# Kernel optimization log

Measured on AMD Instinct MI355X. Metric: run time of the kernel, lower is better.

The kernel has to match this reference:

```python
import jax, jax.numpy as jnp
import numpy as np

# Model/config dims (Llama-3-8B style attention, GQA 32q/8kv)
B, S, HID = 4, 512, 4096
NH, NKV, D = 32, 8, 128
CAP = 2048          # KV cache capacity
MAXPOS = 2048       # max_position_embeddings
START = 1024        # kvcache_start_index (uniform across batch -> static masking)
EPS = 1e-6
QK_SCALE = 1.0 / float(D) ** 0.5
NEG = -1e9


def setup_inputs() -> dict:
    key = jax.random.key(0)
    ks = jax.random.split(key, 8)
    w = 0.02  # weight init scale
    return {
        'hidden_states': jax.random.normal(ks[0], (B, S, HID), jnp.float32),
        'k_cache': jax.random.normal(ks[1], (B, NKV, CAP, D), jnp.float32),
        'v_cache': jax.random.normal(ks[2], (B, NKV, CAP, D), jnp.float32),
        'rope_rotary_cos_sin': jax.random.uniform(ks[3], (B, MAXPOS, D), jnp.float32),
        'context_lengths': jnp.full((B,), S, jnp.int32),
        'kvcache_start_index': jnp.full((B,), START, jnp.int32),
        'Wq': jax.random.normal(ks[4], (HID, NH * D), jnp.float32) * w,
        'Wk': jax.random.normal(ks[5], (HID, NKV * D), jnp.float32) * w,
        'Wv': jax.random.normal(ks[6], (HID, NKV * D), jnp.float32) * w,
        'Wo': jax.random.normal(ks[7], (NH * D, HID), jnp.float32) * w,
        'q_norm_w': jnp.ones((D,), jnp.float32),
        'k_norm_w': jnp.ones((D,), jnp.float32),
    }


def _rmsnorm(x, w):
    # per-head RMSNorm over head_dim (Qwen3-style QK norm)
    return x * jax.lax.rsqrt(jnp.mean(x * x, axis=-1, keepdims=True) + EPS) * w


def _apply_rope(x, cos, sin, pos):
    # x: [B,H,S,D]; cos/sin: [MAXPOS, D/2]; pos: [B,S]
    c = cos[pos][:, None, :, :]  # [B,1,S,D/2]
    s = sin[pos][:, None, :, :]
    x1, x2 = jnp.split(x, 2, axis=-1)
    return jnp.concatenate([x1 * c - x2 * s, x2 * c + x1 * s], axis=-1)


def reference(hidden_states, k_cache, v_cache, rope_rotary_cos_sin,
              context_lengths, kvcache_start_index,
              Wq, Wk, Wv, Wo, q_norm_w, k_norm_w):
    b, s, _ = hidden_states.shape
    # fused QKV projection
    q = (hidden_states @ Wq).reshape(b, s, NH, D)
    k = (hidden_states @ Wk).reshape(b, s, NKV, D)
    v = (hidden_states @ Wv).reshape(b, s, NKV, D)
    # QK norm
    q = _rmsnorm(q, q_norm_w)
    k = _rmsnorm(k, k_norm_w)
    # [B,H,S,D]
    q = q.transpose(0, 2, 1, 3)
    k = k.transpose(0, 2, 1, 3)
    v = v.transpose(0, 2, 1, 3)
    # RoPE tables: first half cos, second half sin; batch dim 0 only
    half = D // 2
    cos = rope_rotary_cos_sin[0, :, :half]
    sin = rope_rotary_cos_sin[0, :, half:]
    pos = kvcache_start_index[:, None] + jnp.arange(s, dtype=kvcache_start_index.dtype)[None, :]
    q = _apply_rope(q, cos, sin, pos)
    k = _apply_rope(k, cos, sin, pos)
    # KV cache update: write new k/v at per-batch start index
    def upd(cache, new, st):  # cache [H,CAP,D], new [H,S,D]
        return jax.lax.dynamic_update_slice(cache, new, (0, st, 0))
    present_k = jax.vmap(upd)(k_cache, k, kvcache_start_index)
    present_v = jax.vmap(upd)(v_cache, v, kvcache_start_index)
    # GQA: expand kv heads to attention heads
    g = NH // NKV
    kf = jnp.repeat(present_k, g, axis=1)  # [B,NH,CAP,D]
    vf = jnp.repeat(present_v, g, axis=1)
    # scaled attention over cache; mask cols beyond absolute query position
    scores = jnp.einsum('bhsd,bhtd->bhst', q * QK_SCALE, kf)
    col = jnp.arange(CAP, dtype=pos.dtype)
    allowed = col[None, None, :] <= pos[:, :, None]        # [B,S,CAP]
    scores = jnp.where(allowed[:, None, :, :], scores, NEG)
    attn = jax.nn.softmax(scores, axis=-1)
    out = jnp.einsum('bhst,bhtd->bhsd', attn, vf)
    out = out.transpose(0, 2, 1, 3).reshape(b, s, NH * D)
    out = out @ Wo
    return out, present_k, present_v
```

## Files before the change

### kernel.cpp

```cpp
#include <hip/hip_runtime.h>
#include <hip/hip_bf16.h>
#include <cstdint>

#define Bsz   4
#define Ssz   512
#define HIDsz 4096
#define NHsz  32
#define NKVsz 8
#define Dsz   128
#define CAPsz 2048
#define EPSf  1e-6f
#define QK_SCALEf 0.08838834764831845f

typedef __attribute__((ext_vector_type(8))) short short8;
typedef __attribute__((ext_vector_type(4))) float f32x4;

__device__ __forceinline__ unsigned short f2bf(float x) {
    unsigned u = __float_as_uint(x);
    return (unsigned short)((u + 0x7fffu + ((u >> 16) & 1u)) >> 16);
}

__device__ __forceinline__ void gload16(const void* g, void* l) {
    __builtin_amdgcn_global_load_lds(
        (const __attribute__((address_space(1))) unsigned int*)g,
        (__attribute__((address_space(3))) unsigned int*)l, 16, 0, 0);
}

__global__ __launch_bounds__(256) void convert_bf16_kernel(
    const float* __restrict__ in, unsigned short* __restrict__ out, int n4)
{
    int i = blockIdx.x * blockDim.x + threadIdx.x;
    if (i < n4) {
        float4 v = ((const float4*)in)[i];
        ushort4 o;
        o.x = f2bf(v.x); o.y = f2bf(v.y); o.z = f2bf(v.z); o.w = f2bf(v.w);
        ((ushort4*)out)[i] = o;
    }
}

__global__ __launch_bounds__(256) void transpose_bf16_kernel(
    const float* __restrict__ W, unsigned short* __restrict__ Wt, int K, int N)
{
    __shared__ float tile[64][65];
    const int k0 = blockIdx.y * 64, n0 = blockIdx.x * 64;
    const int t = threadIdx.x;
    const int tr = t >> 4, tc4 = (t & 15) * 4;
#pragma unroll
    for (int i = 0; i < 4; i++) {
        int r = tr + i * 16;
        float4 v = *(const float4*)(W + (size_t)(k0 + r) * N + n0 + tc4);
        tile[r][tc4 + 0] = v.x; tile[r][tc4 + 1] = v.y;
        tile[r][tc4 + 2] = v.z; tile[r][tc4 + 3] = v.w;
    }
    __syncthreads();
#pragma unroll
    for (int i = 0; i < 4; i++) {
        int nr = tr + i * 16;
        ushort4 o;
        o.x = f2bf(tile[tc4 + 0][nr]);
        o.y = f2bf(tile[tc4 + 1][nr]);
        o.z = f2bf(tile[tc4 + 2][nr]);
        o.w = f2bf(tile[tc4 + 3][nr]);
        *(ushort4*)(Wt + (size_t)(n0 + nr) * K + k0 + tc4) = o;
    }
}

__global__ __launch_bounds__(256) void transpose_v_kernel(
    const float* __restrict__ V, unsigned short* __restrict__ Vt)
{
    __shared__ float tile[64][65];
    const int c0 = blockIdx.x * 64, d0 = blockIdx.y * 64, bk = blockIdx.z;
    const int t = threadIdx.x;
    const int tr = t >> 4, tc4 = (t & 15) * 4;
    const float* base = V + (size_t)bk * CAPsz * Dsz;
#pragma unroll
    for (int i = 0; i < 4; i++) {
        int r = tr + i * 16;
        float4 v = *(const float4*)(base + (size_t)(c0 + r) * Dsz + d0 + tc4);
        tile[r][tc4 + 0] = v.x; tile[r][tc4 + 1] = v.y;
        tile[r][tc4 + 2] = v.z; tile[r][tc4 + 3] = v.w;
    }
    __syncthreads();
    unsigned short* ob = Vt + (size_t)bk * Dsz * CAPsz;
#pragma unroll
    for (int i = 0; i < 4; i++) {
        int dr = tr + i * 16;
        ushort4 o;
        o.x = f2bf(tile[tc4 + 0][dr]);
        o.y = f2bf(tile[tc4 + 1][dr]);
        o.z = f2bf(tile[tc4 + 2][dr]);
        o.w = f2bf(tile[tc4 + 3][dr]);
        *(ushort4*)(ob + (size_t)(d0 + dr) * CAPsz + c0 + tc4) = o;
    }
}

__global__ __launch_bounds__(256, 2) void gemm_bf16_kernel(
    const unsigned short* __restrict__ A,
    const unsigned short* __restrict__ Bt,
    float* __restrict__ C, int M, int N, int K)
{
    __shared__ __align__(16) unsigned short As[128 * 64];
    __shared__ __align__(16) unsigned short Bs[128 * 64];
    const int t    = threadIdx.x;
    const int lane = t & 63, wv = t >> 6;
    const int m0 = blockIdx.y * 128, n0 = blockIdx.x * 128;
    const int rw = (wv & 1) * 64, cw = (wv >> 1) * 64;

    f32x4 acc[4][4];
#pragma unroll
    for (int r = 0; r < 4; r++)
#pragma unroll
        for (int c = 0; c < 4; c++) acc[r][c] = (f32x4){0.f, 0.f, 0.f, 0.f};

    const int arow = lane >> 3;
    const int acol = (lane & 7) * 8;
    const int fr = lane & 15, fq = (lane >> 4) * 8;

    for (int k0 = 0; k0 < K; k0 += 64) {
        __syncthreads();
#pragma unroll
        for (int i = 0; i < 4; i++) {
            int ro = (i * 4 + wv) * 8;
            gload16(A  + (size_t)(m0 + ro + arow) * K + k0 + acol, As + (size_t)ro * 64);
            gload16(Bt + (size_t)(n0 + ro + arow) * K + k0 + acol, Bs + (size_t)ro * 64);
        }
        __syncthreads();
#pragma unroll
        for (int kk = 0; kk < 2; kk++) {
            short8 af[4], bfr[4];
#pragma unroll
            for (int r = 0; r < 4; r++)
                af[r] = *(const short8*)&As[(rw + r * 16 + fr) * 64 + kk * 32 + fq];
#pragma unroll
            for (int c = 0; c < 4; c++)
                bfr[c] = *(const short8*)&Bs[(cw + c * 16 + fr) * 64 + kk * 32 + fq];
#pragma unroll
            for (int r = 0; r < 4; r++)
#pragma unroll
                for (int c = 0; c < 4; c++)
                    acc[r][c] = __builtin_amdgcn_mfma_f32_16x16x32_bf16(
                        af[r], bfr[c], acc[r][c], 0, 0, 0);
        }
    }

#pragma unroll
    for (int r = 0; r < 4; r++) {
#pragma unroll
        for (int c = 0; c < 4; c++) {
            int col = n0 + cw + c * 16 + (lane & 15);
#pragma unroll
            for (int reg = 0; reg < 4; reg++) {
                int row = m0 + rw + r * 16 + (lane >> 4) * 4 + reg;
                C[(size_t)row * N + col] = acc[r][c][reg];
            }
        }
    }
}

__global__ __launch_bounds__(256, 2) void gemm_qkv_kernel(
    const unsigned short* __restrict__ A,
    const unsigned short* __restrict__ Bt,
    float* __restrict__ Cq,
    float* __restrict__ Ck,
    float* __restrict__ Cv,
    const int* __restrict__ start_idx)
{
    __shared__ __align__(16) unsigned short As[128 * 64];
    __shared__ __align__(16) unsigned short Bs[128 * 64];
    const int t    = threadIdx.x;
    const int lane = t & 63, wv = t >> 6;
    const int m0 = blockIdx.y * 128, n0 = blockIdx.x * 128;
    const int rw = (wv & 1) * 64, cw = (wv >> 1) * 64;

    f32x4 acc[4][4];
#pragma unroll
    for (int r = 0; r < 4; r++)
#pragma unroll
        for (int c = 0; c < 4; c++) acc[r][c] = (f32x4){0.f, 0.f, 0.f, 0.f};

    const int arow = lane >> 3;
    const int acol = (lane & 7) * 8;
    const int fr = lane & 15, fq = (lane >> 4) * 8;

    for (int k0 = 0; k0 < HIDsz; k0 += 64) {
        __syncthreads();
#pragma unroll
        for (int i = 0; i < 4; i++) {
            int ro = (i * 4 + wv) * 8;
            gload16(A  + (size_t)(m0 + ro + arow) * HIDsz + k0 + acol, As + (size_t)ro * 64);
            gload16(Bt + (size_t)(n0 + ro + arow) * HIDsz + k0 + acol, Bs + (size_t)ro * 64);
        }
        __syncthreads();
#pragma unroll
        for (int kk = 0; kk < 2; kk++) {
            short8 af[4], bfr[4];
#pragma unroll
            for (int r = 0; r < 4; r++)
                af[r] = *(const short8*)&As[(rw + r * 16 + fr) * 64 + kk * 32 + fq];
#pragma unroll
            for (int c = 0; c < 4; c++)
                bfr[c] = *(const short8*)&Bs[(cw + c * 16 + fr) * 64 + kk * 32 + fq];
#pragma unroll
            for (int r = 0; r < 4; r++)
#pragma unroll
                for (int c = 0; c < 4; c++)
                    acc[r][c] = __builtin_amdgcn_mfma_f32_16x16x32_bf16(
                        af[r], bfr[c], acc[r][c], 0, 0, 0);
        }
    }

    const int pos0 = start_idx[m0 >> 9];
    const bool isQ = (n0 < 4096);
    const bool isK = (n0 >= 4096) && (n0 < 5120);
    float* dst = isK ? Ck : Cv;
    const int cbase = isK ? 4096 : 5120;
#pragma unroll
    for (int r = 0; r < 4; r++) {
#pragma unroll
        for (int c = 0; c < 4; c++) {
            int col = n0 + cw + c * 16 + (lane & 15);
#pragma unroll
            for (int reg = 0; reg < 4; reg++) {
                int row = m0 + rw + r * 16 + (lane >> 4) * 4 + reg;
                float val = acc[r][c][reg];
                if (isQ) {
                    Cq[(size_t)row * 4096 + col] = val;
                } else {
                    int cc = col - cbase;
                    int pos = pos0 + (row & (Ssz - 1));
                    int b = row >> 9;
                    dst[((size_t)(b * NKVsz + (cc >> 7)) * CAPsz + pos) * Dsz + (cc & 127)] = val;
                }
            }
        }
    }
}

__global__ __launch_bounds__(256) void rmsnorm_rope_kernel(
    float* __restrict__ X, unsigned short* __restrict__ Xbf,
    const float* __restrict__ w,
    const float* __restrict__ rope, const int* __restrict__ start_idx,
    int nheads, int mode)
{
    int gid   = blockIdx.x * blockDim.x + threadIdx.x;
    int wid   = gid >> 6;
    int lane  = threadIdx.x & 63;
    int token = wid / nheads;
    int h     = wid - token * nheads;
    int b = token >> 9, s = token & (Ssz - 1);
    int pos = start_idx[b] + s;
    float* row;
    if (mode == 0) row = X + (size_t)token * (nheads * Dsz) + h * Dsz;
    else           row = X + ((size_t)(b * nheads + h) * CAPsz + pos) * Dsz;

    float x1 = row[lane], x2 = row[lane + 64];
    float ss = x1 * x1 + x2 * x2;
#pragma unroll
    for (int off = 32; off > 0; off >>= 1) ss += __shfl_xor(ss, off);
    float rn  = rsqrtf(ss * (1.f / 128.f) + EPSf);
    float xn1 = x1 * rn * w[lane];
    float xn2 = x2 * rn * w[lane + 64];
    float c   = rope[(size_t)pos * Dsz + lane];
    float sn  = rope[(size_t)pos * Dsz + 64 + lane];
    float o1 = xn1 * c - xn2 * sn;
    float o2 = xn2 * c + xn1 * sn;
    if (mode == 0) {
        unsigned short* orow = Xbf + (size_t)token * (nheads * Dsz) + h * Dsz;
        orow[lane]      = f2bf(o1 * QK_SCALEf);
        orow[lane + 64] = f2bf(o2 * QK_SCALEf);
    } else {
        row[lane]      = o1;
        row[lane + 64] = o2;
    }
}

__global__ __launch_bounds__(256, 2) void attn_mfma_kernel(
    const unsigned short* __restrict__ Qbf,
    const unsigned short* __restrict__ Kbf,
    const unsigned short* __restrict__ Vtbf,
    unsigned short* __restrict__ O,
    const int* __restrict__ start_idx)
{
    __shared__ __align__(16) unsigned short Ks[64 * 128];
    __shared__ __align__(16) unsigned short Vs[128 * 64];
    __shared__ __align__(16) unsigned short Ps[4][32 * 72];

    const int t = threadIdx.x, lane = t & 63, wv = t >> 6;
    const int l15 = lane & 15, l4 = lane >> 4;
    const int qt = blockIdx.x, kv = blockIdx.y, b = blockIdx.z;
    const int h = kv * 4 + wv;
    const int s0 = qt * 32;
    const int start = start_idx[b];

    const int swz = (l15 & 7) << 3;

    short8 aq[2][4];
    const unsigned short* qb = Qbf + ((size_t)(b * Ssz + s0)) * HIDsz + h * Dsz;
#pragma unroll
    for (int m2 = 0; m2 < 2; m2++)
#pragma unroll
        for (int kq = 0; kq < 4; kq++)
            aq[m2][kq] = *(const short8*)(qb + (size_t)(m2 * 16 + l15) * HIDsz + kq * 32 + l4 * 8);

    f32x4 Oacc[2][8];
    float m_run[2][4], l_run[2][4];
#pragma unroll
    for (int m2 = 0; m2 < 2; m2++) {
#pragma unroll
        for (int nd = 0; nd < 8; nd++) Oacc[m2][nd] = (f32x4){0.f, 0.f, 0.f, 0.f};
#pragma unroll
        for (int r = 0; r < 4; r++) { m_run[m2][r] = -1e30f; l_run[m2][r] = 0.f; }
    }

    const unsigned short* kb = Kbf + (size_t)(b * NKVsz + kv) * CAPsz * Dsz;
    const unsigned short* vb = Vtbf + (size_t)(b * NKVsz + kv) * (size_t)Dsz * CAPsz;

    int t_hi = start + s0 + 31;
    if (t_hi > CAPsz - 1) t_hi = CAPsz - 1;

    int krow[4], vrow[4];
    unsigned short* kw[4];
    unsigned short* vw[4];
#pragma unroll
    for (int i = 0; i < 4; i++) {
        int kr = (i * 4 + wv) * 4 + l4;
        krow[i] = kr;
        kw[i] = &Ks[kr * 128 + ((l15 * 8) ^ ((kr & 7) << 3))];
        int vr = (i * 4 + wv) * 8 + (lane >> 3);
        vrow[i] = vr;
        vw[i] = &Vs[vr * 64 + (((lane & 7) * 8) ^ ((vr & 7) << 3))];
    }

    short8 kreg[4], vreg[4];
#pragma unroll
    for (int i = 0; i < 4; i++) {
        kreg[i] = *(const short8*)(kb + (size_t)krow[i] * Dsz + l15 * 8);
        vreg[i] = *(const short8*)(vb + (size_t)vrow[i] * CAPsz + (lane & 7) * 8);
    }

    for (int t0 = 0; t0 <= t_hi; t0 += 64) {
        asm volatile("s_waitcnt lgkmcnt(0)" ::: "memory");
        __builtin_amdgcn_s_barrier();
        __builtin_amdgcn_sched_barrier(0);

#pragma unroll
        for (int i = 0; i < 4; i++) *(short8*)kw[i] = kreg[i];
#pragma unroll
        for (int i = 0; i < 4; i++) *(short8*)vw[i] = vreg[i];

        if (t0 + 64 <= t_hi) {
            int tn = t0 + 64;
#pragma unroll
            for (int i = 0; i < 4; i++) {
                kreg[i] = *(const short8*)(kb + (size_t)(tn + krow[i]) * Dsz + l15 * 8);
                vreg[i] = *(const short8*)(vb + (size_t)vrow[i] * CAPsz + tn + (lane & 7) * 8);
            }
        }

        asm volatile("s_waitcnt lgkmcnt(0)" ::: "memory");
        __builtin_amdgcn_s_barrier();
        __builtin_amdgcn_sched_barrier(0);

        f32x4 Sacc[2][4];
#pragma unroll
        for (int m2 = 0; m2 < 2; m2++)
#pragma unroll
            for (int n = 0; n < 4; n++) Sacc[m2][n] = (f32x4){0.f, 0.f, 0.f, 0.f};
        __builtin_amdgcn_s_setprio(1);
#pragma unroll
        for (int kq = 0; kq < 4; kq++) {
            short8 bk[4];
#pragma unroll
            for (int n = 0; n < 4; n++)
                bk[n] = *(const short8*)&Ks[(n * 16 + l15) * 128 + ((kq * 32 + l4 * 8) ^ swz)];
#pragma unroll
            for (int m2 = 0; m2 < 2; m2++)
#pragma unroll
                for (int n = 0; n < 4; n++)
                    Sacc[m2][n] = __builtin_amdgcn_mfma_f32_16x16x32_bf16(
                        aq[m2][kq], bk[n], Sacc[m2][n], 0, 0, 0);
        }
        __builtin_amdgcn_s_setprio(0);

        bool need_mask = (t0 + 63) > (start + s0);
#pragma unroll
        for (int m2 = 0; m2 < 2; m2++) {
#pragma unroll
            for (int reg = 0; reg < 4; reg++) {
                int rloc = m2 * 16 + l4 * 4 + reg;
                int row_pos = start + s0 + rloc;
                float sv[4];
#pragma unroll
                for (int n = 0; n < 4; n++) {
                    sv[n] = Sacc[m2][n][reg];
                    if (need_mask && (t0 + n * 16 + l15 > row_pos)) sv[n] = -1e30f;
                }
                float mrow = fmaxf(fmaxf(sv[0], sv[1]), fmaxf(sv[2], sv[3]));
#pragma unroll
                for (int off = 1; off < 16; off <<= 1)
                    mrow = fmaxf(mrow, __shfl_xor(mrow, off));
                float m_new = fmaxf(m_run[m2][reg], mrow);
                float alpha = __expf(m_run[m2][reg] - m_new);
                float ps = 0.f;
#pragma unroll
                for (int n = 0; n < 4; n++) {
                    sv[n] = __expf(sv[n] - m_new);
                    ps += sv[n];
                }
#pragma unroll
                for (int off = 1; off < 16; off <<= 1)
                    ps += __shfl_xor(ps, off);
                l_run[m2][reg] = l_run[m2][reg] * alpha + ps;
                m_run[m2][reg] = m_new;
#pragma unroll
                for (int nd = 0; nd < 8; nd++) Oacc[m2][nd][reg] *= alpha;
#pragma unroll
                for (int n = 0; n < 4; n++)
                    Ps[wv][rloc * 72 + n * 16 + l15] = f2bf(sv[n]);
            }
        }

        __builtin_amdgcn_s_setprio(1);
#pragma unroll
        for (int kp = 0; kp < 2; kp++) {
            short8 ap[2];
#pragma unroll
            for (int m2 = 0; m2 < 2; m2++)
                ap[m2] = *(const short8*)&Ps[wv][(m2 * 16 + l15) * 72 + kp * 32 + l4 * 8];
#pragma unroll
            for (int nd = 0; nd < 8; nd++) {
                short8 bv = *(const short8*)&Vs[(nd * 16 + l15) * 64 + ((kp * 32 + l4 * 8) ^ swz)];
#pragma unroll
                for (int m2 = 0; m2 < 2; m2++)
                    Oacc[m2][nd] = __builtin_amdgcn_mfma_f32_16x16x32_bf16(
                        ap[m2], bv, Oacc[m2][nd], 0, 0, 0);
            }
        }
        __builtin_amdgcn_s_setprio(0);
    }

    unsigned short* ob = O + ((size_t)(b * Ssz + s0)) * HIDsz + h * Dsz;
#pragma unroll
    for (int m2 = 0; m2 < 2; m2++)
#pragma unroll
        for (int reg = 0; reg < 4; reg++) {
            int rloc = m2 * 16 + l4 * 4 + reg;
            float inv = 1.f / l_run[m2][reg];
#pragma unroll
            for (int nd = 0; nd < 8; nd++)
                ob[(size_t)rloc * HIDsz + nd * 16 + l15] = f2bf(Oacc[m2][nd][reg] * inv);
        }
}

extern "C" void kernel_launch(void* const* d_in, const int* in_sizes, int n_in,
                              void* d_out, int out_size, void* d_ws, size_t ws_size,
                              hipStream_t stream) {
    (void)in_sizes; (void)n_in; (void)out_size; (void)ws_size;
    const float* hidden    = (const float*)d_in[0];
    const float* k_cache   = (const float*)d_in[1];
    const float* v_cache   = (const float*)d_in[2];
    const float* rope      = (const float*)d_in[3];
    const int*   start_idx = (const int*)d_in[5];
    const float* Wq        = (const float*)d_in[6];
    const float* Wk        = (const float*)d_in[7];
    const float* Wv        = (const float*)d_in[8];
    const float* Wo        = (const float*)d_in[9];
    const float* q_norm_w  = (const float*)d_in[10];
    const float* k_norm_w  = (const float*)d_in[11];

    float* out   = (float*)d_out;
    float* out_k = out + (size_t)Bsz * Ssz * HIDsz;
    float* out_v = out_k + (size_t)Bsz * NKVsz * CAPsz * Dsz;

    char* ws = (char*)d_ws;
    float*          q_ws      = (float*)ws;
    unsigned short* Kbf       = (unsigned short*)ws;
    unsigned short* Vtbf      = (unsigned short*)(ws + (((size_t) 16) << 20));
    unsigned short* hidden_bf = (unsigned short*)(ws + (((size_t) 32) << 20));
    unsigned short* attn_bf   = (unsigned short*)(ws + (((size_t) 48) << 20));
    unsigned short* qbf       = (unsigned short*)(ws + (((size_t) 64) << 20));
    unsigned short* Wqkv_t    = (unsigned short*)(ws + (((size_t) 80) << 20));
    unsigned short* Wk_t      = Wqkv_t + (size_t)4096 * 4096;
    unsigned short* Wv_t      = Wqkv_t + (size_t)5120 * 4096;
    unsigned short* Wo_t      = Wqkv_t;

    const size_t cache_bytes = (size_t)Bsz * NKVsz * CAPsz * Dsz * sizeof(float);
    (void)hipMemcpyAsync(out_k, k_cache, cache_bytes, hipMemcpyDeviceToDevice, stream);
    (void)hipMemcpyAsync(out_v, v_cache, cache_bytes, hipMemcpyDeviceToDevice, stream);

    convert_bf16_kernel<<<8192, 256, 0, stream>>>(hidden, hidden_bf, 2048 * 4096 / 4);
    transpose_bf16_kernel<<<dim3(64, 64), 256, 0, stream>>>(Wq, Wqkv_t, HIDsz, NHsz * Dsz);
    transpose_bf16_kernel<<<dim3(16, 64), 256, 0, stream>>>(Wk, Wk_t, HIDsz, NKVsz * Dsz);
    transpose_bf16_kernel<<<dim3(16, 64), 256, 0, stream>>>(Wv, Wv_t, HIDsz, NKVsz * Dsz);

    gemm_qkv_kernel<<<dim3(48, 16), 256, 0, stream>>>(
        hidden_bf, Wqkv_t, q_ws, out_k, out_v, start_idx);

    rmsnorm_rope_kernel<<<16384, 256, 0, stream>>>(q_ws, qbf, q_norm_w, rope, start_idx, NHsz, 0);
    rmsnorm_rope_kernel<<<4096, 256, 0, stream>>>(out_k, nullptr, k_norm_w, rope, start_idx, NKVsz, 1);

    convert_bf16_kernel<<<8192, 256, 0, stream>>>(out_k, Kbf, Bsz * NKVsz * CAPsz * Dsz / 4);
    transpose_v_kernel<<<dim3(32, 2, 32), 256, 0, stream>>>(out_v, Vtbf);

    attn_mfma_kernel<<<dim3(16, NKVsz, Bsz), 256, 0, stream>>>(qbf, Kbf, Vtbf, attn_bf, start_idx);

    transpose_bf16_kernel<<<dim3(64, 64), 256, 0, stream>>>(Wo, Wo_t, NHsz * Dsz, HIDsz);
    gemm_bf16_kernel<<<dim3(32, 16), 256, 0, stream>>>(attn_bf, Wo_t, out, 2048, 4096, 4096);
}
```

Before: 673.3 us.

## Fuse QK RMSNorm and RoPE into QKV GEMM epilogue, skip unused cache regions

Moves the per-head RMSNorm and RoPE for Q and K into the QKV GEMM epilogue. A shared-memory reduction produces the row norms, and RoPE partners are swapped between waves through shared memory. Q is written directly as bf16 and K as both fp32 and bf16, which removes the fp32 Q round trip and the separate norm/rope kernels. The K bf16 conversion and the V transpose now skip cache positions the attention does not read, and the three weight transposes are merged into one launch. Occupancy hints are raised to 3 blocks. The epilogue now uses more shared memory and extra syncs, which may limit the higher occupancy target.

```diff
diff --git a/kernel.cpp b/kernel.cpp
--- a/kernel.cpp
+++ b/kernel.cpp
@@ -38,6 +38,20 @@
     }
 }
 
+__global__ __launch_bounds__(256) void convert_k_prefix_kernel(
+    const float* __restrict__ in, unsigned short* __restrict__ out,
+    const int* __restrict__ start_idx)
+{
+    int i = blockIdx.x * blockDim.x + threadIdx.x;
+    int pos = (i >> 5) & (CAPsz - 1);
+    int b   = i >> 19;
+    if (pos >= start_idx[b]) return;
+    float4 v = ((const float4*)in)[i];
+    ushort4 o;
+    o.x = f2bf(v.x); o.y = f2bf(v.y); o.z = f2bf(v.z); o.w = f2bf(v.w);
+    ((ushort4*)out)[i] = o;
+}
+
 __global__ __launch_bounds__(256) void transpose_bf16_kernel(
     const float* __restrict__ W, unsigned short* __restrict__ Wt, int K, int N)
 {
@@ -65,11 +79,47 @@
     }
 }
 
+__global__ __launch_bounds__(256) void transpose_wqkv_kernel(
+    const float* __restrict__ Wq, const float* __restrict__ Wk,
+    const float* __restrict__ Wv, unsigned short* __restrict__ Wt)
+{
+    __shared__ float tile[64][65];
+    const int nt = blockIdx.x;
+    const int k0 = blockIdx.y * 64;
+    const float* W; int srcN, c0;
+    if (nt < 64)      { W = Wq; srcN = 4096; c0 = nt * 64; }
+    else if (nt < 80) { W = Wk; srcN = 1024; c0 = (nt - 64) * 64; }
+    else              { W = Wv; srcN = 1024; c0 = (nt - 80) * 64; }
+    const int t = threadIdx.x;
+    const int tr = t >> 4, tc4 = (t & 15) * 4;
+#pragma unroll
+    for (int i = 0; i < 4; i++) {
+        int r = tr + i * 16;
+        float4 v = *(const float4*)(W + (size_t)(k0 + r) * srcN + c0 + tc4);
+        tile[r][tc4 + 0] = v.x; tile[r][tc4 + 1] = v.y;
+        tile[r][tc4 + 2] = v.z; tile[r][tc4 + 3] = v.w;
+    }
+    __syncthreads();
+    const int n0 = nt * 64;
+#pragma unroll
+    for (int i = 0; i < 4; i++) {
+        int nr = tr + i * 16;
+        ushort4 o;
+        o.x = f2bf(tile[tc4 + 0][nr]);
+        o.y = f2bf(tile[tc4 + 1][nr]);
+        o.z = f2bf(tile[tc4 + 2][nr]);
+        o.w = f2bf(tile[tc4 + 3][nr]);
+        *(ushort4*)(Wt + (size_t)(n0 + nr) * HIDsz + k0 + tc4) = o;
+    }
+}
+
 __global__ __launch_bounds__(256) void transpose_v_kernel(
-    const float* __restrict__ V, unsigned short* __restrict__ Vt)
+    const float* __restrict__ V, unsigned short* __restrict__ Vt,
+    const int* __restrict__ start_idx)
 {
     __shared__ float tile[64][65];
     const int c0 = blockIdx.x * 64, d0 = blockIdx.y * 64, bk = blockIdx.z;
+    if (c0 >= start_idx[bk >> 3] + Ssz) return;
     const int t = threadIdx.x;
     const int tr = t >> 4, tc4 = (t & 15) * 4;
     const float* base = V + (size_t)bk * CAPsz * Dsz;
@@ -94,7 +144,7 @@
     }
 }
 
-__global__ __launch_bounds__(256, 2) void gemm_bf16_kernel(
+__global__ __launch_bounds__(256, 3) void gemm_bf16_kernel(
     const unsigned short* __restrict__ A,
     const unsigned short* __restrict__ Bt,
     float* __restrict__ C, int M, int N, int K)
@@ -157,20 +207,27 @@
     }
 }
 
-__global__ __launch_bounds__(256, 2) void gemm_qkv_kernel(
+__global__ __launch_bounds__(256, 3) void gemm_qkv_kernel(
     const unsigned short* __restrict__ A,
     const unsigned short* __restrict__ Bt,
-    float* __restrict__ Cq,
+    unsigned short* __restrict__ Qout,
     float* __restrict__ Ck,
     float* __restrict__ Cv,
+    unsigned short* __restrict__ Kbf,
+    const float* __restrict__ rope,
+    const float* __restrict__ qw,
+    const float* __restrict__ knw,
     const int* __restrict__ start_idx)
 {
     __shared__ __align__(16) unsigned short As[128 * 64];
     __shared__ __align__(16) unsigned short Bs[128 * 64];
+    __shared__ float ssbuf[256];
+    __shared__ float xbuf[256 * 17];
     const int t    = threadIdx.x;
     const int lane = t & 63, wv = t >> 6;
     const int m0 = blockIdx.y * 128, n0 = blockIdx.x * 128;
     const int rw = (wv & 1) * 64, cw = (wv >> 1) * 64;
+    const int l15 = lane & 15, l4 = lane >> 4;
 
     f32x4 acc[4][4];
 #pragma unroll
@@ -180,7 +237,7 @@
 
     const int arow = lane >> 3;
     const int acol = (lane & 7) * 8;
-    const int fr = lane & 15, fq = (lane >> 4) * 8;
+    const int fr = l15, fq = l4 * 8;
 
     for (int k0 = 0; k0 < HIDsz; k0 += 64) {
         __syncthreads();
@@ -209,68 +266,101 @@
         }
     }
 
-    const int pos0 = start_idx[m0 >> 9];
+    const int m0b  = m0 & (Ssz - 1);
+    const int bat  = m0 >> 9;
+    const int pos0 = start_idx[bat];
+
+    if (n0 >= 5120) {
+#pragma unroll
+        for (int r = 0; r < 4; r++) {
+#pragma unroll
+            for (int c = 0; c < 4; c++) {
+                int cc = (n0 - 5120) + cw + c * 16 + l15;
+                int kvh = cc >> 7, d = cc & 127;
+#pragma unroll
+                for (int reg = 0; reg < 4; reg++) {
+                    int srow = rw + r * 16 + l4 * 4 + reg;
+                    int pos = pos0 + m0b + srow;
+                    Cv[((size_t)(bat * NKVsz + kvh) * CAPsz + pos) * Dsz + d] = acc[r][c][reg];
+                }
+            }
+        }
+        return;
+    }
+
     const bool isQ = (n0 < 4096);
-    const bool isK = (n0 >= 4096) && (n0 < 5120);
-    float* dst = isK ? Ck : Cv;
-    const int cbase = isK ? 4096 : 5120;
+    const float* w = isQ ? qw : knw;
+
+#pragma unroll
+    for (int r = 0; r < 4; r++)
+#pragma unroll
+        for (int reg = 0; reg < 4; reg++) {
+            float p = acc[r][0][reg] * acc[r][0][reg]
+                    + acc[r][1][reg] * acc[r][1][reg]
+                    + acc[r][2][reg] * acc[r][2][reg]
+                    + acc[r][3][reg] * acc[r][3][reg];
+#pragma unroll
+            for (int off = 1; off < 16; off <<= 1) p += __shfl_xor(p, off);
+            if (l15 == 0)
+                ssbuf[(rw + r * 16 + l4 * 4 + reg) * 2 + (cw >> 6)] = p;
+        }
+    __syncthreads();
+
+    float wv4[4];
+#pragma unroll
+    for (int c = 0; c < 4; c++) wv4[c] = w[cw + c * 16 + l15];
+
+    float rn[4][4];
+#pragma unroll
+    for (int r = 0; r < 4; r++)
+#pragma unroll
+        for (int reg = 0; reg < 4; reg++) {
+            int srow = rw + r * 16 + l4 * 4 + reg;
+            rn[r][reg] = rsqrtf((ssbuf[srow * 2] + ssbuf[srow * 2 + 1]) * (1.f / 128.f) + EPSf);
+        }
+
+    const int kvh = isQ ? 0 : ((n0 - 4096) >> 7);
+
 #pragma unroll
     for (int r = 0; r < 4; r++) {
-#pragma unroll
-        for (int c = 0; c < 4; c++) {
-            int col = n0 + cw + c * 16 + (lane & 15);
+        float xn[4][4];
+#pragma unroll
+        for (int c = 0; c < 4; c++)
 #pragma unroll
             for (int reg = 0; reg < 4; reg++) {
-                int row = m0 + rw + r * 16 + (lane >> 4) * 4 + reg;
-                float val = acc[r][c][reg];
+                xn[c][reg] = acc[r][c][reg] * rn[r][reg] * wv4[c];
+                xbuf[t * 17 + c * 4 + reg] = xn[c][reg];
+            }
+        __syncthreads();
+        float xp[4][4];
+#pragma unroll
+        for (int c = 0; c < 4; c++)
+#pragma unroll
+            for (int reg = 0; reg < 4; reg++)
+                xp[c][reg] = xbuf[(t ^ 128) * 17 + c * 4 + reg];
+
+#pragma unroll
+        for (int reg = 0; reg < 4; reg++) {
+            int srow = rw + r * 16 + l4 * 4 + reg;
+            int pos = pos0 + m0b + srow;
+            const float* rb = rope + (size_t)pos * Dsz;
+#pragma unroll
+            for (int c = 0; c < 4; c++) {
+                int dh = cw + c * 16 + l15;
+                int j = dh & 63;
+                float co = rb[j], si = rb[64 + j];
+                float o = (cw == 0) ? xn[c][reg] * co - xp[c][reg] * si
+                                    : xn[c][reg] * co + xp[c][reg] * si;
                 if (isQ) {
-                    Cq[(size_t)row * 4096 + col] = val;
+                    Qout[(size_t)(m0 + srow) * 4096 + n0 + dh] = f2bf(o * QK_SCALEf);
                 } else {
-                    int cc = col - cbase;
-                    int pos = pos0 + (row & (Ssz - 1));
-                    int b = row >> 9;
-                    dst[((size_t)(b * NKVsz + (cc >> 7)) * CAPsz + pos) * Dsz + (cc & 127)] = val;
+                    size_t off = ((size_t)(bat * NKVsz + kvh) * CAPsz + pos) * Dsz + dh;
+                    Ck[off]  = o;
+                    Kbf[off] = f2bf(o);
                 }
             }
         }
-    }
-}
-
-__global__ __launch_bounds__(256) void rmsnorm_rope_kernel(
-    float* __restrict__ X, unsigned short* __restrict__ Xbf,
-    const float* __restrict__ w,
-    const float* __restrict__ rope, const int* __restrict__ start_idx,
-    int nheads, int mode)
-{
-    int gid   = blockIdx.x * blockDim.x + threadIdx.x;
-    int wid   = gid >> 6;
-    int lane  = threadIdx.x & 63;
-    int token = wid / nheads;
-    int h     = wid - token * nheads;
-    int b = token >> 9, s = token & (Ssz - 1);
-    int pos = start_idx[b] + s;
-    float* row;
-    if (mode == 0) row = X + (size_t)token * (nheads * Dsz) + h * Dsz;
-    else           row = X + ((size_t)(b * nheads + h) * CAPsz + pos) * Dsz;
-
-    float x1 = row[lane], x2 = row[lane + 64];
-    float ss = x1 * x1 + x2 * x2;
-#pragma unroll
-    for (int off = 32; off > 0; off >>= 1) ss += __shfl_xor(ss, off);
-    float rn  = rsqrtf(ss * (1.f / 128.f) + EPSf);
-    float xn1 = x1 * rn * w[lane];
-    float xn2 = x2 * rn * w[lane + 64];
-    float c   = rope[(size_t)pos * Dsz + lane];
-    float sn  = rope[(size_t)pos * Dsz + 64 + lane];
-    float o1 = xn1 * c - xn2 * sn;
-    float o2 = xn2 * c + xn1 * sn;
-    if (mode == 0) {
-        unsigned short* orow = Xbf + (size_t)token * (nheads * Dsz) + h * Dsz;
-        orow[lane]      = f2bf(o1 * QK_SCALEf);
-        orow[lane + 64] = f2bf(o2 * QK_SCALEf);
-    } else {
-        row[lane]      = o1;
-        row[lane + 64] = o2;
+        __syncthreads();
     }
 }
 
@@ -473,15 +563,12 @@
     float* out_v = out_k + (size_t)Bsz * NKVsz * CAPsz * Dsz;
 
     char* ws = (char*)d_ws;
-    float*          q_ws      = (float*)ws;
     unsigned short* Kbf       = (unsigned short*)ws;
     unsigned short* Vtbf      = (unsigned short*)(ws + (((size_t) 16) << 20));
     unsigned short* hidden_bf = (unsigned short*)(ws + (((size_t) 32) << 20));
     unsigned short* attn_bf   = (unsigned short*)(ws + (((size_t) 48) << 20));
     unsigned short* qbf       = (unsigned short*)(ws + (((size_t) 64) << 20));
     unsigned short* Wqkv_t    = (unsigned short*)(ws + (((size_t) 80) << 20));
-    unsigned short* Wk_t      = Wqkv_t + (size_t)4096 * 4096;
-    unsigned short* Wv_t      = Wqkv_t + (size_t)5120 * 4096;
     unsigned short* Wo_t      = Wqkv_t;
 
     const size_t cache_bytes = (size_t)Bsz * NKVsz * CAPsz * Dsz * sizeof(float);
@@ -489,18 +576,14 @@
     (void)hipMemcpyAsync(out_v, v_cache, cache_bytes, hipMemcpyDeviceToDevice, stream);
 
     convert_bf16_kernel<<<8192, 256, 0, stream>>>(hidden, hidden_bf, 2048 * 4096 / 4);
-    transpose_bf16_kernel<<<dim3(64, 64), 256, 0, stream>>>(Wq, Wqkv_t, HIDsz, NHsz * Dsz);
-    transpose_bf16_kernel<<<dim3(16, 64), 256, 0, stream>>>(Wk, Wk_t, HIDsz, NKVsz * Dsz);
-    transpose_bf16_kernel<<<dim3(16, 64), 256, 0, stream>>>(Wv, Wv_t, HIDsz, NKVsz * Dsz);
+    transpose_wqkv_kernel<<<dim3(96, 64), 256, 0, stream>>>(Wq, Wk, Wv, Wqkv_t);
 
     gemm_qkv_kernel<<<dim3(48, 16), 256, 0, stream>>>(
-        hidden_bf, Wqkv_t, q_ws, out_k, out_v, start_idx);
-
-    rmsnorm_rope_kernel<<<16384, 256, 0, stream>>>(q_ws, qbf, q_norm_w, rope, start_idx, NHsz, 0);
-    rmsnorm_rope_kernel<<<4096, 256, 0, stream>>>(out_k, nullptr, k_norm_w, rope, start_idx, NKVsz, 1);
-
-    convert_bf16_kernel<<<8192, 256, 0, stream>>>(out_k, Kbf, Bsz * NKVsz * CAPsz * Dsz / 4);
-    transpose_v_kernel<<<dim3(32, 2, 32), 256, 0, stream>>>(out_v, Vtbf);
+        hidden_bf, Wqkv_t, qbf, out_k, out_v, Kbf, rope,
+        q_norm_w, k_norm_w, start_idx);
+
+    convert_k_prefix_kernel<<<8192, 256, 0, stream>>>(out_k, Kbf, start_idx);
+    transpose_v_kernel<<<dim3(32, 2, 32), 256, 0, stream>>>(out_v, Vtbf, start_idx);
 
     attn_mfma_kernel<<<dim3(16, NKVsz, Bsz), 256, 0, stream>>>(qbf, Kbf, Vtbf, attn_bf, start_idx);
 
```

Result: no change. 662.3 us (-1.6%).
